# Kernel optimization log

Hardware: AMD Instinct MI355X
Metric: run time of the kernel (lower is better)

Reference implementation:

```python
import jax, jax.numpy as jnp
import numpy as np

H = 12          # num_heads
D = 32          # head_dim = dim // num_heads
C = H * D       # 384
SCALE = D ** -0.5


def _split2(y, B, N):
    # y: [B, N, 2*C] -> two tensors [B, H, N, D] (branch 1, branch 2)
    y = y.reshape(B, N, 2, H, D)
    return y[:, :, 0].transpose(0, 2, 1, 3), y[:, :, 1].transpose(0, 2, 1, 3)


def setup_inputs() -> dict:
    key = jax.random.key(0)
    ks = jax.random.split(key, 16)
    s = 0.02
    inp = {
        "x": jax.random.normal(ks[0], (8, 4096, C), jnp.float32),
        "attn": jax.random.normal(ks[1], (8, 4096, C), jnp.float32),
        "agent_input": jax.random.normal(ks[2], (8, 64, C), jnp.float32),
        # Linear weights stored as [in, out] (jax convention)
        "Wq_lf": jax.random.normal(ks[3], (C, 2 * C), jnp.float32) * s,
        "bq_lf": jnp.zeros((2 * C,), jnp.float32),
        "Wk_ag": jax.random.normal(ks[4], (C, 2 * C), jnp.float32) * s,
        "bk_ag": jnp.zeros((2 * C,), jnp.float32),
        "wa": jax.random.normal(ks[5], (2,), jnp.float32) * 0.5,   # mlp_attn_a Linear(2,1) weight
        "ba": jnp.zeros((1,), jnp.float32),
        "Wq_ag": jax.random.normal(ks[6], (C, 2 * C), jnp.float32) * s,
        "bq_ag": jnp.zeros((2 * C,), jnp.float32),
        "Wk_hf": jax.random.normal(ks[7], (C, 2 * C), jnp.float32) * s,
        "bk_hf": jnp.zeros((2 * C,), jnp.float32),
        "Wv_hf": jax.random.normal(ks[8], (C, C), jnp.float32) * s,
        "bv_hf": jnp.zeros((C,), jnp.float32),
        "wb": jax.random.normal(ks[9], (2,), jnp.float32) * 0.5,   # mlp_attn_b Linear(2,1) weight
        "bb": jnp.zeros((1,), jnp.float32),
        "Wproj": jax.random.normal(ks[10], (C, C), jnp.float32) * s,
        "bproj": jnp.zeros((C,), jnp.float32),
    }
    return inp


def reference(x, attn, agent_input, Wq_lf, bq_lf, Wk_ag, bk_ag, wa, ba,
              Wq_ag, bq_ag, Wk_hf, bk_hf, Wv_hf, bv_hf, wb, bb, Wproj, bproj):
    B, N, _ = x.shape
    Na = agent_input.shape[1]
    # --- branch A: pixel queries vs agent keys ---
    q1, q2 = _split2(x @ Wq_lf + bq_lf, B, N)              # [B,H,N,D] x2
    k1, k2 = _split2(agent_input @ Wk_ag + bk_ag, B, Na)   # [B,H,Na,D] x2
    s1 = jnp.einsum('bhnd,bhmd->bhnm', q1, k1) * SCALE     # [B,H,N,Na]
    s2 = jnp.einsum('bhnd,bhmd->bhnm', q2, k2) * SCALE
    # Linear(2,1) fusion of stacked scores, then softmax over agents
    attn_agent = jax.nn.softmax(s1 * wa[0] + s2 * wa[1] + ba[0], axis=-1)
    # --- branch B: agent queries vs high-freq keys/values ---
    qa1, qa2 = _split2(agent_input @ Wq_ag + bq_ag, B, Na)  # [B,H,Na,D] x2
    kh1, kh2 = _split2(attn @ Wk_hf + bk_hf, B, N)          # [B,H,N,D] x2
    v = (attn @ Wv_hf + bv_hf).reshape(B, N, H, D).transpose(0, 2, 1, 3)  # [B,H,N,D]
    t1 = jnp.einsum('bhmd,bhnd->bhmn', qa1, kh1) * SCALE    # [B,H,Na,N]
    t2 = jnp.einsum('bhmd,bhnd->bhmn', qa2, kh2) * SCALE
    attn_v = jax.nn.softmax(t1 * wb[0] + t2 * wb[1] + bb[0], axis=-1)
    x_s = attn_v @ v                 # [B,H,Na,D]
    x_out = attn_agent @ x_s         # [B,H,N,D]
    x_out = x_out.transpose(0, 2, 1, 3).reshape(B, N, H * D)
    return x_out @ Wproj + bproj
```

## Files before the change

kernel.cpp:

```cpp
#include <hip/hip_runtime.h>

#define KB 8
#define KN 4096
#define KNA 64
#define KH 12
#define KD 32
#define KC 384
#define KC2 768
#define KSCALE 0.17677669529663688f
#define NCH 16

typedef __bf16 bf16x8 __attribute__((ext_vector_type(8)));
typedef float  f32x4  __attribute__((ext_vector_type(4)));

static __device__ __forceinline__ unsigned short f2bf(float f) {
    unsigned int u = __builtin_bit_cast(unsigned int, f);
    u += 0x7FFFu + ((u >> 16) & 1u);
    return (unsigned short)(u >> 16);
}
static __device__ __forceinline__ float bf2f(unsigned short h) {
    return __builtin_bit_cast(float, (unsigned int)h << 16);
}

static __device__ __forceinline__ void gld_lds16(const unsigned short* g, unsigned short* l) {
    __builtin_amdgcn_global_load_lds(
        (const __attribute__((address_space(1))) unsigned int*)g,
        (__attribute__((address_space(3))) unsigned int*)l, 16, 0, 0);
}

#define MFMA_16x16x32 __builtin_amdgcn_mfma_f32_16x16x32_bf16

__global__ __launch_bounds__(256) void k_transpose(
    const float* __restrict__ Win, float* __restrict__ Wout)
{
    __shared__ float tile[32][33];
    const int tx = threadIdx.x, ty = threadIdx.y;
    const int j0 = blockIdx.x * 32, c0 = blockIdx.y * 32;
    #pragma unroll
    for (int yy = 0; yy < 4; ++yy)
        tile[ty + yy*8][tx] = Win[(size_t)(c0 + ty + yy*8)*KC2 + j0 + tx];
    __syncthreads();
    #pragma unroll
    for (int yy = 0; yy < 4; ++yy)
        Wout[(size_t)(j0 + ty + yy*8)*KC + c0 + tx] = tile[tx][ty + yy*8];
}

__global__ __launch_bounds__(256) void k_tcastT(
    const float* __restrict__ src, unsigned short* __restrict__ dstT,
    unsigned short* __restrict__ dstRM,
    int R, int C, long sstride, long dTstride, long dRMstride)
{
    __shared__ unsigned short lds[64][80];
    const int t = threadIdx.x;
    const int r0 = blockIdx.x * 64, c0 = blockIdx.y * 64;
    const float* s = src + (size_t)blockIdx.z * sstride;
    #pragma unroll
    for (int i = 0; i < 16; ++i) {
        int f = t + i*256; int rr = f >> 6, cc = f & 63;
        lds[rr][cc] = f2bf(s[(size_t)(r0+rr)*C + c0 + cc]);
    }
    __syncthreads();
    if (dstT) {
        unsigned short* dT = dstT + (size_t)blockIdx.z * dTstride;
        #pragma unroll
        for (int i = 0; i < 8; ++i) {
            int o = t + i*256;
            int chunk = o >> 10, c = (o >> 4) & 63, pair = o & 15;
            int r = chunk*32 + pair*2;
            unsigned int v = (unsigned int)lds[r][c] | ((unsigned int)lds[r+1][c] << 16);
            size_t off = ((size_t)((r0>>5) + chunk)*C + c0 + c)*32 + pair*2;
            *reinterpret_cast<unsigned int*>(dT + off) = v;
        }
    }
    if (dstRM) {
        unsigned short* dR = dstRM + (size_t)blockIdx.z * dRMstride;
        #pragma unroll
        for (int i = 0; i < 2; ++i) {
            int idx = t*2 + i;
            int n = idx >> 3, gt = idx & 7;
            int g = (c0 >> 3) + gt;
            int slot = g ^ ((r0 + n) & 7);
            *reinterpret_cast<bf16x8*>(dR + (size_t)(r0+n)*C + slot*8) =
                *reinterpret_cast<const bf16x8*>(&lds[n][gt*8]);
        }
    }
}

__global__ __launch_bounds__(256) void k_tcastHL(
    const float* __restrict__ src, unsigned short* __restrict__ dstHi,
    unsigned short* __restrict__ dstLo)
{
    __shared__ unsigned short lh[64][80];
    __shared__ unsigned short ll[64][80];
    const int t = threadIdx.x;
    const int r0 = blockIdx.x * 64, c0 = blockIdx.y * 64;
    #pragma unroll
    for (int i = 0; i < 16; ++i) {
        int f = t + i*256; int rr = f >> 6, cc = f & 63;
        float v = src[(size_t)(r0+rr)*KC2 + c0 + cc];
        unsigned short h = f2bf(v);
        lh[rr][cc] = h;
        ll[rr][cc] = f2bf(v - bf2f(h));
    }
    __syncthreads();
    #pragma unroll
    for (int i = 0; i < 8; ++i) {
        int o = t + i*256;
        int chunk = o >> 10, c = (o >> 4) & 63, pair = o & 15;
        int r = chunk*32 + pair*2;
        unsigned int vh = (unsigned int)lh[r][c] | ((unsigned int)lh[r+1][c] << 16);
        unsigned int vl = (unsigned int)ll[r][c] | ((unsigned int)ll[r+1][c] << 16);
        size_t off = ((size_t)((r0>>5) + chunk)*KC2 + c0 + c)*32 + pair*2;
        *reinterpret_cast<unsigned int*>(dstHi + off) = vh;
        *reinterpret_cast<unsigned int*>(dstLo + off) = vl;
    }
}

__global__ __launch_bounds__(512, 1) void k_agproj2(
    const float* __restrict__ agent,
    const unsigned short* __restrict__ KHi, const unsigned short* __restrict__ KLo,
    const unsigned short* __restrict__ QHi, const unsigned short* __restrict__ QLo,
    const float* __restrict__ bk_ag, const float* __restrict__ bq_ag,
    float* __restrict__ Kag, float* __restrict__ Qa)
{
    extern __shared__ char smem[];
    unsigned short* aHi = (unsigned short*)smem;
    unsigned short* aLo = (unsigned short*)(smem + 49152);
    const int tid = threadIdx.x;
    const int wid = tid >> 6, lane = tid & 63;
    const int tx = lane & 15, ty = lane >> 4;
    const int rt = blockIdx.x, wsel = blockIdx.y, z = blockIdx.z;
    const unsigned short* WHi = wsel ? QHi : KHi;
    const unsigned short* WLo = wsel ? QLo : KLo;
    const float* bias = wsel ? bq_ag : bk_ag;
    float* dst = wsel ? Qa : Kag;

    {
        const float4* s4 = reinterpret_cast<const float4*>(agent + (size_t)rt*64*KC);
        #pragma unroll
        for (int i = 0; i < 12; ++i) {
            int f = tid + i*512;
            int n = f / 96, c4 = f % 96;
            float4 v = s4[f];
            ushort4 h4, l4;
            h4.x = f2bf(v.x); l4.x = f2bf(v.x - bf2f(h4.x));
            h4.y = f2bf(v.y); l4.y = f2bf(v.y - bf2f(h4.y));
            h4.z = f2bf(v.z); l4.z = f2bf(v.z - bf2f(h4.z));
            h4.w = f2bf(v.w); l4.w = f2bf(v.w - bf2f(h4.w));
            int g = c4 >> 1, half = c4 & 1;
            int gs = g ^ (n & 7);
            *reinterpret_cast<ushort4*>(aHi + n*384 + gs*8 + half*4) = h4;
            *reinterpret_cast<ushort4*>(aLo + n*384 + gs*8 + half*4) = l4;
        }
    }
    f32x4 acc[4][3];
    #pragma unroll
    for (int i = 0; i < 4; ++i)
        #pragma unroll
        for (int j = 0; j < 3; ++j) acc[i][j] = (f32x4){0.f,0.f,0.f,0.f};
    __syncthreads();

    #pragma unroll
    for (int kk = 0; kk < 12; ++kk) {
        bf16x8 ah[4], al[4];
        #pragma unroll
        for (int ng = 0; ng < 4; ++ng) {
            int n = ng*16 + tx;
            int gs = (kk*4 + ty) ^ (n & 7);
            ah[ng] = *reinterpret_cast<const bf16x8*>(aHi + n*384 + gs*8);
            al[ng] = *reinterpret_cast<const bf16x8*>(aLo + n*384 + gs*8);
        }
        #pragma unroll
        for (int cs = 0; cs < 3; ++cs) {
            int col = z*KC + wid*48 + cs*16 + tx;
            bf16x8 bh = *reinterpret_cast<const bf16x8*>(WHi + ((size_t)kk*KC2 + col)*32 + ty*8);
            bf16x8 bl = *reinterpret_cast<const bf16x8*>(WLo + ((size_t)kk*KC2 + col)*32 + ty*8);
            #pragma unroll
            for (int ng = 0; ng < 4; ++ng) {
                acc[ng][cs] = MFMA_16x16x32(ah[ng], bh, acc[ng][cs], 0, 0, 0);
                acc[ng][cs] = MFMA_16x16x32(ah[ng], bl, acc[ng][cs], 0, 0, 0);
                acc[ng][cs] = MFMA_16x16x32(al[ng], bh, acc[ng][cs], 0, 0, 0);
            }
        }
    }
    #pragma unroll
    for (int cs = 0; cs < 3; ++cs) {
        int col = z*KC + wid*48 + cs*16 + tx;
        float bv = bias[col];
        #pragma unroll
        for (int ng = 0; ng < 4; ++ng)
            #pragma unroll
            for (int r = 0; r < 4; ++r) {
                int row = rt*64 + ng*16 + ty*4 + r;
                dst[(size_t)row*KC2 + col] = acc[ng][cs][r] + bv;
            }
    }
}

__global__ __launch_bounds__(128) void k_build_F(
    const float* __restrict__ WkT, const float* __restrict__ Qa,
    const float* __restrict__ wb, unsigned short* __restrict__ Fbf)
{
    __shared__ float q_lds[8][64];
    const int tid = threadIdx.x;
    const int g = blockIdx.x;
    const int b = blockIdx.y;
    const int h = (g*8) >> 6;
    const float t0 = KSCALE*wb[0], t1 = KSCALE*wb[1];
    #pragma unroll
    for (int l = 0; l < 4; ++l) {
        int v = tid + l*128;
        int i = v >> 6, d = v & 63;
        int m = (g*8 + i) & 63;
        int jj = (d < KD) ? (h*KD + d) : (KC + h*KD + d - KD);
        float cf = (d < KD) ? t0 : t1;
        q_lds[i][d] = cf * Qa[(size_t)(b*KNA + m)*KC2 + jj];
    }
    __syncthreads();
    float acc[8][3] = {};
    for (int d = 0; d < 64; ++d) {
        int row = (d < KD) ? (h*KD + d) : (KC + h*KD + d - KD);
        const float* wr = WkT + (size_t)row*KC;
        float w0 = wr[tid], w1 = wr[tid+128], w2 = wr[tid+256];
        #pragma unroll
        for (int i = 0; i < 8; ++i) {
            float q = q_lds[i][d];
            acc[i][0] = fmaf(q, w0, acc[i][0]);
            acc[i][1] = fmaf(q, w1, acc[i][1]);
            acc[i][2] = fmaf(q, w2, acc[i][2]);
        }
    }
    #pragma unroll
    for (int i = 0; i < 8; ++i)
        #pragma unroll
        for (int l = 0; l < 3; ++l)
            Fbf[((size_t)b*KC2 + g*8 + i)*KC + tid + l*128] = f2bf(acc[i][l]);
}

__global__ __launch_bounds__(256) void k_kabc(
    const float* __restrict__ Kag, const float* __restrict__ Qa,
    const float* __restrict__ wa, const float* __restrict__ bk_hf,
    const float* __restrict__ wb, const float* __restrict__ bbv,
    unsigned short* __restrict__ KA, float* __restrict__ cB)
{
    const int b = blockIdx.x, tid = threadIdx.x;
    const float s0 = KSCALE * wa[0], s1 = KSCALE * wa[1];
    #pragma unroll
    for (int i = 0; i < 24; ++i) {
        int v = tid + i*256;
        int w = v >> 8, m = (v >> 2) & 63, k8 = v & 3;
        float sc = (w >= 12) ? s1 : s0;
        const float* sp = Kag + ((size_t)(b*KNA + m))*KC2 + w*32 + k8*8;
        float4 f0 = *reinterpret_cast<const float4*>(sp);
        float4 f1 = *reinterpret_cast<const float4*>(sp + 4);
        ushort4 h0 = { f2bf(f0.x*sc), f2bf(f0.y*sc), f2bf(f0.z*sc), f2bf(f0.w*sc) };
        ushort4 h1 = { f2bf(f1.x*sc), f2bf(f1.y*sc), f2bf(f1.z*sc), f2bf(f1.w*sc) };
        unsigned short* dp = KA + ((size_t)(b*24 + w)*64 + m)*32 + k8*8;
        *reinterpret_cast<ushort4*>(dp)     = h0;
        *reinterpret_cast<ushort4*>(dp + 4) = h1;
    }
    const float t0 = KSCALE*wb[0], t1 = KSCALE*wb[1];
    for (int hm = tid; hm < KC2; hm += 256) {
        int h = hm >> 6, m = hm & 63;
        const float* qp = Qa + (size_t)(b*KNA + m)*KC2;
        float bb2 = 0.f;
        for (int d = 0; d < KD; ++d)
            bb2 += t0*bk_hf[h*KD+d]*qp[h*KD+d] + t1*bk_hf[KC+h*KD+d]*qp[KC+h*KD+d];
        cB[(size_t)b*KC2 + hm] = bb2 + bbv[0];
    }
}

__global__ __launch_bounds__(512, 4) void k_vproj2(
    const float* __restrict__ attn, const unsigned short* __restrict__ WvT2,
    const float* __restrict__ bv, unsigned short* __restrict__ Abf,
    unsigned short* __restrict__ Vt2)
{
    extern __shared__ char smem[];
    unsigned short* a_rm = (unsigned short*)smem;
    const int tid = threadIdx.x;
    const int wid = tid >> 6, lane = tid & 63;
    const int tx = lane & 15, ty = lane >> 4;
    const int nb = blockIdx.x, b = blockIdx.y;
    const int wn = wid >> 2, wd = wid & 3;

    {
        const float4* src = reinterpret_cast<const float4*>(attn + ((size_t)(b*KN + nb*64))*KC);
        unsigned short* ab = Abf + ((size_t)(b*KN + nb*64))*KC;
        #pragma unroll
        for (int i = 0; i < 12; ++i) {
            int f = tid + i*512;
            int n = f / 96, c4 = f % 96;
            float4 v = src[f];
            ushort4 h4 = { f2bf(v.x), f2bf(v.y), f2bf(v.z), f2bf(v.w) };
            int g = c4 >> 1, half = c4 & 1;
            int gs = g ^ (n & 7);
            *reinterpret_cast<ushort4*>(a_rm + n*384 + gs*8 + half*4) = h4;
            *reinterpret_cast<ushort4*>(ab + (size_t)n*384 + gs*8 + half*4) = h4;
        }
    }
    f32x4 acc[2][6];
    #pragma unroll
    for (int i = 0; i < 2; ++i)
        #pragma unroll
        for (int j = 0; j < 6; ++j) acc[i][j] = (f32x4){0.f,0.f,0.f,0.f};
    __syncthreads();

    #pragma unroll
    for (int kk = 0; kk < 12; ++kk) {
        bf16x8 af[2];
        #pragma unroll
        for (int ns = 0; ns < 2; ++ns) {
            int n = wn*32 + ns*16 + tx;
            int gs = (kk*4 + ty) ^ (n & 7);
            af[ns] = *reinterpret_cast<const bf16x8*>(a_rm + n*384 + gs*8);
        }
        #pragma unroll
        for (int cs = 0; cs < 6; ++cs) {
            int d = wd*96 + cs*16 + tx;
            bf16x8 bf = *reinterpret_cast<const bf16x8*>(WvT2 + ((size_t)kk*KC + d)*32 + ty*8);
            #pragma unroll
            for (int ns = 0; ns < 2; ++ns)
                acc[ns][cs] = MFMA_16x16x32(af[ns], bf, acc[ns][cs], 0, 0, 0);
        }
    }
    #pragma unroll
    for (int cs = 0; cs < 6; ++cs) {
        int d = wd*96 + cs*16 + tx;
        float bvv = bv[d];
        #pragma unroll
        for (int ns = 0; ns < 2; ++ns) {
            ushort4 h4;
            h4.x = f2bf(acc[ns][cs][0] + bvv);
            h4.y = f2bf(acc[ns][cs][1] + bvv);
            h4.z = f2bf(acc[ns][cs][2] + bvv);
            h4.w = f2bf(acc[ns][cs][3] + bvv);
            size_t off = (((size_t)b*(KN>>5) + nb*2 + wn)*KC + d)*32 + ns*16 + ty*4;
            *reinterpret_cast<ushort4*>(Vt2 + off) = h4;
        }
    }
}

__global__ __launch_bounds__(512, 4) void k_flash3(
    const unsigned short* __restrict__ Abf, const unsigned short* __restrict__ Vt2,
    const unsigned short* __restrict__ Fbf, const float* __restrict__ cB,
    float* __restrict__ Vpart, float* __restrict__ lpart,
    int nchunk, int NK)
{
    extern __shared__ char smem[];
    unsigned short* a_rm = (unsigned short*)smem;
    unsigned short* p    = (unsigned short*)(smem + 49152);
    float*          redl = (float*)(smem + 58368);

    const int tid = threadIdx.x;
    const int wid = tid >> 6, lane = tid & 63;
    const int tx = lane & 15, ty = lane >> 4;
    const unsigned bid = blockIdx.x;
    const unsigned g = bid / KH;
    const int h = bid - g*KH;
    const int b = g / nchunk;
    const int chunk = g - b*nchunk;
    const int n0 = chunk * NK;
    const int wn = wid >> 2, wh = wid & 3;
    const int wph = wid >> 1, wpd = wid & 1;

    bf16x8 ffrag[12];
    {
        const unsigned short* fp = Fbf + ((size_t)(b*KC2 + h*64 + wh*16 + tx))*KC + ty*8;
        #pragma unroll
        for (int kk = 0; kk < 12; ++kk)
            ffrag[kk] = *reinterpret_cast<const bf16x8*>(fp + kk*32);
    }
    const float cbv = cB[(size_t)b*KC2 + h*64 + wh*16 + tx];
    float lacc = 0.f;
    f32x4 Vacc = (f32x4){0.f,0.f,0.f,0.f};

    const unsigned short* atile = Abf + ((size_t)b*KN + n0)*KC;
    #pragma unroll
    for (int i = 0; i < 6; ++i)
        gld_lds16(atile + (size_t)tid*8 + i*4096, a_rm + tid*8 + i*4096);
    __syncthreads();

    const int NT = NK >> 6;
    for (int nt = 0; nt < NT; ++nt) {
        size_t vrow = (size_t)b*(KN >> 5) + ((n0 + nt*64) >> 5);
        bf16x8 vf0 = *reinterpret_cast<const bf16x8*>(
            Vt2 + ((vrow + 0)*KC + h*KD + wpd*16 + tx)*32 + ty*8);
        bf16x8 vf1 = *reinterpret_cast<const bf16x8*>(
            Vt2 + ((vrow + 1)*KC + h*KD + wpd*16 + tx)*32 + ty*8);
        f32x4 tacc[2];
        tacc[0] = (f32x4){0.f,0.f,0.f,0.f};
        tacc[1] = (f32x4){0.f,0.f,0.f,0.f};
        __builtin_amdgcn_s_setprio(1);
        #pragma unroll
        for (int kk = 0; kk < 12; ++kk) {
            #pragma unroll
            for (int ns = 0; ns < 2; ++ns) {
                int n = wn*32 + ns*16 + tx;
                int gs = (kk*4 + ty) ^ (n & 7);
                bf16x8 af = *reinterpret_cast<const bf16x8*>(a_rm + n*384 + gs*8);
                tacc[ns] = MFMA_16x16x32(af, ffrag[kk], tacc[ns], 0, 0, 0);
            }
        }
        __builtin_amdgcn_s_setprio(0);
        #pragma unroll
        for (int ns = 0; ns < 2; ++ns) {
            float e0 = __expf(tacc[ns][0] + cbv);
            float e1 = __expf(tacc[ns][1] + cbv);
            float e2 = __expf(tacc[ns][2] + cbv);
            float e3 = __expf(tacc[ns][3] + cbv);
            lacc += e0 + e1 + e2 + e3;
            int hm = wh*16 + tx;
            int np = wn*32 + ns*16 + ty*4;
            ushort4 h4 = { f2bf(e0), f2bf(e1), f2bf(e2), f2bf(e3) };
            *reinterpret_cast<ushort4*>(p + hm*72 + np) = h4;
        }
        __syncthreads();
        if (nt + 1 < NT) {
            const unsigned short* at = atile + (size_t)(nt+1)*64*KC;
            #pragma unroll
            for (int i = 0; i < 6; ++i)
                gld_lds16(at + (size_t)tid*8 + i*4096, a_rm + tid*8 + i*4096);
        }
        bf16x8 pa0 = *reinterpret_cast<const bf16x8*>(p + (wph*16 + tx)*72 + 0*32 + ty*8);
        bf16x8 pa1 = *reinterpret_cast<const bf16x8*>(p + (wph*16 + tx)*72 + 1*32 + ty*8);
        Vacc = MFMA_16x16x32(pa0, vf0, Vacc, 0, 0, 0);
        Vacc = MFMA_16x16x32(pa1, vf1, Vacc, 0, 0, 0);
        __syncthreads();
    }
    #pragma unroll
    for (int r = 0; r < 4; ++r)
        Vpart[(((size_t)(b*KH + h)*nchunk + chunk)*64 + wph*16 + ty*4 + r)*32 + wpd*16 + tx]
            = Vacc[r];
    lacc += __shfl_xor(lacc, 16);
    lacc += __shfl_xor(lacc, 32);
    if (lane < 16) redl[wn*64 + wh*16 + tx] = lacc;
    __syncthreads();
    if (tid < 64)
        lpart[((size_t)b*KC2 + h*64 + tid)*nchunk + chunk] = redl[tid] + redl[64 + tid];
}

__global__ __launch_bounds__(384) void k_combine4(
    const float* __restrict__ Vpart, const float* __restrict__ lpart,
    const float* __restrict__ Wproj, unsigned short* __restrict__ Mt2)
{
    __shared__ float xs[16][32];
    __shared__ float lred[16][NCH];
    __shared__ float invl[16];
    const int h = blockIdx.x, b = blockIdx.y, q = blockIdx.z;
    const int tid = threadIdx.x;
    if (tid < 16*NCH) {
        int hm_l = tid >> 4, ch = tid & (NCH-1);
        lred[hm_l][ch] = lpart[((size_t)b*KC2 + h*64 + q*16 + hm_l)*NCH + ch];
    }
    __syncthreads();
    if (tid < 16) {
        float s = 0.f;
        #pragma unroll
        for (int j = 0; j < NCH; ++j) s += lred[tid][j];
        invl[tid] = 1.f / s;
    }
    __syncthreads();
    for (int v = tid; v < 512; v += 384) {
        int hm_l = v >> 5, d = v & 31;
        const float* vp = Vpart + (((size_t)(b*KH + h)*NCH)*64 + q*16 + hm_l)*32 + d;
        float u = 0.f;
        #pragma unroll
        for (int ch = 0; ch < NCH; ++ch) u += vp[(size_t)ch*2048];
        xs[hm_l][d] = u * invl[hm_l];
    }
    __syncthreads();
    const int e = tid;
    float wp[32];
    #pragma unroll
    for (int d = 0; d < 32; ++d) wp[d] = Wproj[(size_t)(h*KD + d)*KC + e];
    ushort4 line[4];
    #pragma unroll
    for (int mq = 0; mq < 4; ++mq) {
        float a4[4];
        #pragma unroll
        for (int mr = 0; mr < 4; ++mr) {
            float a = 0.f;
            #pragma unroll
            for (int d = 0; d < 32; ++d)
                a = fmaf(xs[mq*4 + mr][d], wp[d], a);
            a4[mr] = a;
        }
        line[mq] = (ushort4){ f2bf(a4[0]), f2bf(a4[1]), f2bf(a4[2]), f2bf(a4[3]) };
    }
    unsigned short* dst = Mt2 + (((size_t)(b*KH + h)*2 + (q >> 1))*KC + e)*32 + (q & 1)*16;
    #pragma unroll
    for (int mq = 0; mq < 4; ++mq)
        *reinterpret_cast<ushort4*>(dst + mq*4) = line[mq];
}

__global__ __launch_bounds__(512, 4) void k_qkproj(
    const float* __restrict__ src, const unsigned short* __restrict__ WT2,
    const float* __restrict__ bias, unsigned short* __restrict__ dstAf)
{
    extern __shared__ char smem[];
    unsigned short* xb = (unsigned short*)smem;
    const int tid = threadIdx.x;
    const int wid = tid >> 6, lane = tid & 63;
    const int tx = lane & 15, ty = lane >> 4;
    const int nb = blockIdx.x, b = blockIdx.y, z = blockIdx.z;

    {
        const float4* s4 = reinterpret_cast<const float4*>(src + ((size_t)(b*KN + nb*64))*KC);
        #pragma unroll
        for (int i = 0; i < 12; ++i) {
            int f = tid + i*512;
            int n = f / 96, c4 = f % 96;
            float4 v = s4[f];
            ushort4 h4 = { f2bf(v.x), f2bf(v.y), f2bf(v.z), f2bf(v.w) };
            int g = c4 >> 1, half = c4 & 1;
            int gs = g ^ (n & 7);
            *reinterpret_cast<ushort4*>(xb + n*384 + gs*8 + half*4) = h4;
        }
    }
    f32x4 acc[4][3];
    #pragma unroll
    for (int i = 0; i < 4; ++i)
        #pragma unroll
        for (int j = 0; j < 3; ++j) acc[i][j] = (f32x4){0.f,0.f,0.f,0.f};
    __syncthreads();

    #pragma unroll
    for (int kk = 0; kk < 12; ++kk) {
        bf16x8 af[4];
        #pragma unroll
        for (int ng = 0; ng < 4; ++ng) {
            int n = ng*16 + tx;
            int gs = (kk*4 + ty) ^ (n & 7);
            af[ng] = *reinterpret_cast<const bf16x8*>(xb + n*384 + gs*8);
        }
        #pragma unroll
        for (int cs = 0; cs < 3; ++cs) {
            int col = z*KC + wid*48 + cs*16 + tx;
            bf16x8 bf = *reinterpret_cast<const bf16x8*>(WT2 + ((size_t)kk*KC2 + col)*32 + ty*8);
            #pragma unroll
            for (int ng = 0; ng < 4; ++ng)
                acc[ng][cs] = MFMA_16x16x32(af[ng], bf, acc[ng][cs], 0, 0, 0);
        }
    }
    #pragma unroll
    for (int cs = 0; cs < 3; ++cs) {
        int col = z*KC + wid*48 + cs*16 + tx;
        float bv = bias[col];
        int w = col >> 5, tyq = (col >> 3) & 3, j = col & 7;
        #pragma unroll
        for (int ng = 0; ng < 4; ++ng) {
            int nt = nb*4 + ng;
            size_t base = ((((size_t)(b*256 + nt)*24 + w)*4 + tyq)*16)*8 + j;
            #pragma unroll
            for (int r = 0; r < 4; ++r) {
                int row = ty*4 + r;
                dstAf[base + (size_t)row*8] = f2bf(acc[ng][cs][r] + bv);
            }
        }
    }
}

__global__ __launch_bounds__(512, 4) void k_out5(
    const unsigned short* __restrict__ QAf, const unsigned short* __restrict__ KA,
    const float* __restrict__ ba, const unsigned short* __restrict__ Mt2,
    const float* __restrict__ bproj, float* __restrict__ out)
{
    extern __shared__ char smem[];
    unsigned short* p0 = (unsigned short*)smem;
    unsigned short* p1 = (unsigned short*)(smem + 17920);

    const int tid = threadIdx.x;
    const int wid = tid >> 6, lane = tid & 63;
    const int tx = lane & 15, ty = lane >> 4;
    const int nb = blockIdx.x, b = blockIdx.y;
    const int hq2 = wid >> 2, wn = wid & 3;
    const int es = wid * 48;
    const float ba0 = ba[0];

    f32x4 oacc[4][3];
    #pragma unroll
    for (int i = 0; i < 4; ++i)
        #pragma unroll
        for (int j = 0; j < 3; ++j) oacc[i][j] = (f32x4){0.f,0.f,0.f,0.f};

    for (int it = 0; it < 6; ++it) {
        unsigned short* pb = (it & 1) ? p1 : p0;
        const int hq = it*2 + hq2;
        const unsigned short* ap = QAf +
            (((size_t)(b*256 + nb*4 + wn)*24 + hq))*512 + (size_t)lane*8;
        bf16x8 a0 = *reinterpret_cast<const bf16x8*>(ap);
        bf16x8 a1 = *reinterpret_cast<const bf16x8*>(ap + 12*512);
        f32x4 tacc[4];
        #pragma unroll
        for (int s = 0; s < 4; ++s) tacc[s] = (f32x4){0.f,0.f,0.f,0.f};
        __builtin_amdgcn_s_setprio(1);
        #pragma unroll
        for (int s = 0; s < 4; ++s) {
            bf16x8 kb0 = *reinterpret_cast<const bf16x8*>(
                KA + ((size_t)(b*24 + hq)*64 + s*16 + tx)*32 + ty*8);
            bf16x8 kb1 = *reinterpret_cast<const bf16x8*>(
                KA + ((size_t)(b*24 + 12 + hq)*64 + s*16 + tx)*32 + ty*8);
            tacc[s] = MFMA_16x16x32(a0, kb0, tacc[s], 0, 0, 0);
            tacc[s] = MFMA_16x16x32(a1, kb1, tacc[s], 0, 0, 0);
        }
        __builtin_amdgcn_s_setprio(0);
        float e[4][4];
        float ls[4] = {0.f, 0.f, 0.f, 0.f};
        #pragma unroll
        for (int s = 0; s < 4; ++s)
            #pragma unroll
            for (int r = 0; r < 4; ++r) {
                e[s][r] = __expf(tacc[s][r] + ba0);
                ls[r] += e[s][r];
            }
        #pragma unroll
        for (int mask = 1; mask < 16; mask <<= 1)
            #pragma unroll
            for (int r = 0; r < 4; ++r)
                ls[r] += __shfl_xor(ls[r], mask);
        float inv[4];
        #pragma unroll
        for (int r = 0; r < 4; ++r) inv[r] = 1.f / ls[r];
        #pragma unroll
        for (int s = 0; s < 4; ++s)
            #pragma unroll
            for (int r = 0; r < 4; ++r) {
                int n = wn*16 + ty*4 + r;
                pb[n*140 + hq2*64 + s*16 + tx] = f2bf(e[s][r] * inv[r]);
            }
        __syncthreads();
        __builtin_amdgcn_s_setprio(1);
        #pragma unroll
        for (int ks = 0; ks < 4; ++ks) {
            const int hM = it*2 + (ks >> 1);
            const int inner = ks & 1;
            bf16x8 pa[4];
            #pragma unroll
            for (int ng = 0; ng < 4; ++ng)
                pa[ng] = *reinterpret_cast<const bf16x8*>(
                    pb + (ng*16 + tx)*140 + ks*32 + ty*8);
            #pragma unroll
            for (int j = 0; j < 3; ++j) {
                bf16x8 mf = *reinterpret_cast<const bf16x8*>(
                    Mt2 + (((size_t)(b*KH + hM)*2 + inner)*KC + es + j*16 + tx)*32 + ty*8);
                #pragma unroll
                for (int ng = 0; ng < 4; ++ng)
                    oacc[ng][j] = MFMA_16x16x32(pa[ng], mf, oacc[ng][j], 0, 0, 0);
            }
        }
        __builtin_amdgcn_s_setprio(0);
    }
    float bp[3];
    #pragma unroll
    for (int j = 0; j < 3; ++j) bp[j] = bproj[es + j*16 + tx];
    #pragma unroll
    for (int ng = 0; ng < 4; ++ng)
        #pragma unroll
        for (int r = 0; r < 4; ++r) {
            size_t base = (size_t)(b*KN + nb*64 + ng*16 + ty*4 + r)*KC;
            #pragma unroll
            for (int j = 0; j < 3; ++j)
                out[base + es + j*16 + tx] = oacc[ng][j][r] + bp[j];
        }
}

extern "C" void kernel_launch(void* const* d_in, const int* in_sizes, int n_in,
                              void* d_out, int out_size, void* d_ws, size_t ws_size,
                              hipStream_t stream) {
    const float* x     = (const float*)d_in[0];
    const float* attn  = (const float*)d_in[1];
    const float* agent = (const float*)d_in[2];
    const float* Wq_lf = (const float*)d_in[3];
    const float* bq_lf = (const float*)d_in[4];
    const float* Wk_ag = (const float*)d_in[5];
    const float* bk_ag = (const float*)d_in[6];
    const float* wa    = (const float*)d_in[7];
    const float* ba    = (const float*)d_in[8];
    const float* Wq_ag = (const float*)d_in[9];
    const float* bq_ag = (const float*)d_in[10];
    const float* Wk_hf = (const float*)d_in[11];
    const float* bk_hf = (const float*)d_in[12];
    const float* Wv_hf = (const float*)d_in[13];
    const float* bv_hf = (const float*)d_in[14];
    const float* wb    = (const float*)d_in[15];
    const float* bb    = (const float*)d_in[16];
    const float* Wproj = (const float*)d_in[17];
    const float* bproj = (const float*)d_in[18];
    float* out = (float*)d_out;
    float* ws  = (float*)d_ws;

    const size_t o_Kag  = 0;
    const size_t o_Qa   = 393216;
    const size_t o_cB   = 792576;
    const size_t o_Fbf  = 798720;
    const size_t o_WkT  = 1978368;
    const size_t o_WvT2 = 2273280;
    const size_t o_WqT2 = 2310144;
    const size_t o_KA   = 2457600;
    const size_t o_Mt2  = 2654208;
    const size_t o_Abf  = 3833856;
    const size_t o_Vt2  = 6979584;
    const size_t o_lp   = 13271040;
    const size_t o_Vp   = 13467648;
    const size_t o_QAf  = 3833856;
    const size_t o_KHi  = o_Abf;
    const size_t o_KLo  = o_Abf + 147456;
    const size_t o_QHi  = o_Abf + 294912;
    const size_t o_QLo  = o_Abf + 442368;
    (void)ws_size; (void)in_sizes; (void)n_in; (void)out_size;

    unsigned short* Fbf  = (unsigned short*)(ws + o_Fbf);
    unsigned short* WvT2 = (unsigned short*)(ws + o_WvT2);
    unsigned short* WqT2 = (unsigned short*)(ws + o_WqT2);
    unsigned short* KA   = (unsigned short*)(ws + o_KA);
    unsigned short* Mt2  = (unsigned short*)(ws + o_Mt2);
    unsigned short* Abf  = (unsigned short*)(ws + o_Abf);
    unsigned short* Vt2  = (unsigned short*)(ws + o_Vt2);
    unsigned short* QAf  = (unsigned short*)(ws + o_QAf);
    unsigned short* KHi  = (unsigned short*)(ws + o_KHi);
    unsigned short* KLo  = (unsigned short*)(ws + o_KLo);
    unsigned short* QHi  = (unsigned short*)(ws + o_QHi);
    unsigned short* QLo  = (unsigned short*)(ws + o_QLo);

    const int ap_lds = 98304;
    const int vp_lds = 49152;
    const int fl_lds = 58880;
    const int qp_lds = 49152;
    const int ko_lds = 35840;
    (void)hipFuncSetAttribute(reinterpret_cast<const void*>(k_agproj2),
                              hipFuncAttributeMaxDynamicSharedMemorySize, ap_lds);
    (void)hipFuncSetAttribute(reinterpret_cast<const void*>(k_vproj2),
                              hipFuncAttributeMaxDynamicSharedMemorySize, vp_lds);
    (void)hipFuncSetAttribute(reinterpret_cast<const void*>(k_flash3),
                              hipFuncAttributeMaxDynamicSharedMemorySize, fl_lds);
    (void)hipFuncSetAttribute(reinterpret_cast<const void*>(k_qkproj),
                              hipFuncAttributeMaxDynamicSharedMemorySize, qp_lds);
    (void)hipFuncSetAttribute(reinterpret_cast<const void*>(k_out5),
                              hipFuncAttributeMaxDynamicSharedMemorySize, ko_lds);

    k_tcastHL<<<dim3(6, 12), 256, 0, stream>>>(Wk_ag, KHi, KLo);
    k_tcastHL<<<dim3(6, 12), 256, 0, stream>>>(Wq_ag, QHi, QLo);
    k_agproj2<<<dim3(8, 2, 2), 512, ap_lds, stream>>>(
        agent, KHi, KLo, QHi, QLo, bk_ag, bq_ag, ws + o_Kag, ws + o_Qa);
    k_transpose<<<dim3(24, 12), dim3(32, 8), 0, stream>>>(Wk_hf, ws + o_WkT);
    k_tcastT<<<dim3(6, 12, 1), 256, 0, stream>>>(Wq_lf, WqT2, nullptr,
                                                 KC, KC2, 0, 0, 0);
    k_tcastT<<<dim3(6, 6, 1), 256, 0, stream>>>(Wv_hf, WvT2, nullptr,
                                                 KC, KC, 0, 0, 0);
    k_kabc<<<dim3(KB), 256, 0, stream>>>(ws + o_Kag, ws + o_Qa, wa, bk_hf, wb, bb,
                                         KA, ws + o_cB);
    k_build_F<<<dim3(96, 8), 128, 0, stream>>>(ws + o_WkT, ws + o_Qa, wb, Fbf);

    k_vproj2<<<dim3(KN/64, KB), 512, vp_lds, stream>>>(attn, WvT2, bv_hf, Abf, Vt2);

    k_flash3<<<dim3(KH * KB * NCH), 512, fl_lds, stream>>>(
        Abf, Vt2, Fbf, ws + o_cB, ws + o_Vp, ws + o_lp, NCH, KN / NCH);
    k_combine4<<<dim3(KH, KB, 4), 384, 0, stream>>>(
        ws + o_Vp, ws + o_lp, Wproj, Mt2);
    k_qkproj<<<dim3(KN/64, KB, 2), 512, qp_lds, stream>>>(x, WqT2, bq_lf, QAf);
    k_out5<<<dim3(KN/64, KB), 512, ko_lds, stream>>>(
        QAf, KA, ba, Mt2, bproj, out);
}
```

Measured before the change: 263.7 us.

## Fuse query projection into output kernel, keep projected queries in LDS

```diff
diff --git a/kernel.cpp b/kernel.cpp
--- a/kernel.cpp
+++ b/kernel.cpp
@@ -493,19 +493,26 @@
         *reinterpret_cast<ushort4*>(dst + mq*4) = line[mq];
 }
 
-__global__ __launch_bounds__(512, 4) void k_qkproj(
-    const float* __restrict__ src, const unsigned short* __restrict__ WT2,
-    const float* __restrict__ bias, unsigned short* __restrict__ dstAf)
+__global__ __launch_bounds__(512, 1) void k_fused(
+    const float* __restrict__ x, const unsigned short* __restrict__ WT2,
+    const float* __restrict__ bq, const unsigned short* __restrict__ KA,
+    const float* __restrict__ ba, const unsigned short* __restrict__ Mt2,
+    const float* __restrict__ bproj, float* __restrict__ out)
 {
     extern __shared__ char smem[];
     unsigned short* xb = (unsigned short*)smem;
+    unsigned short* p0 = (unsigned short*)smem;
+    unsigned short* p1 = (unsigned short*)(smem + 17920);
+    unsigned short* qf = (unsigned short*)(smem + 49152);
+
     const int tid = threadIdx.x;
     const int wid = tid >> 6, lane = tid & 63;
     const int tx = lane & 15, ty = lane >> 4;
-    const int nb = blockIdx.x, b = blockIdx.y, z = blockIdx.z;
+    const int nb = blockIdx.x, b = blockIdx.y;
+    const float ba0 = ba[0];
 
     {
-        const float4* s4 = reinterpret_cast<const float4*>(src + ((size_t)(b*KN + nb*64))*KC);
+        const float4* s4 = reinterpret_cast<const float4*>(x + ((size_t)(b*KN + nb*64))*KC);
         #pragma unroll
         for (int i = 0; i < 12; ++i) {
             int f = tid + i*512;
@@ -517,65 +524,51 @@
             *reinterpret_cast<ushort4*>(xb + n*384 + gs*8 + half*4) = h4;
         }
     }
-    f32x4 acc[4][3];
-    #pragma unroll
-    for (int i = 0; i < 4; ++i)
-        #pragma unroll
-        for (int j = 0; j < 3; ++j) acc[i][j] = (f32x4){0.f,0.f,0.f,0.f};
-    __syncthreads();
-
-    #pragma unroll
-    for (int kk = 0; kk < 12; ++kk) {
-        bf16x8 af[4];
-        #pragma unroll
-        for (int ng = 0; ng < 4; ++ng) {
-            int n = ng*16 + tx;
-            int gs = (kk*4 + ty) ^ (n & 7);
-            af[ng] = *reinterpret_cast<const bf16x8*>(xb + n*384 + gs*8);
+    __syncthreads();
+
+    #pragma unroll
+    for (int z = 0; z < 2; ++z) {
+        f32x4 acc[4][3];
+        #pragma unroll
+        for (int i = 0; i < 4; ++i)
+            #pragma unroll
+            for (int j = 0; j < 3; ++j) acc[i][j] = (f32x4){0.f,0.f,0.f,0.f};
+        #pragma unroll
+        for (int kk = 0; kk < 12; ++kk) {
+            bf16x8 af[4];
+            #pragma unroll
+            for (int ng = 0; ng < 4; ++ng) {
+                int n = ng*16 + tx;
+                int gs = (kk*4 + ty) ^ (n & 7);
+                af[ng] = *reinterpret_cast<const bf16x8*>(xb + n*384 + gs*8);
+            }
+            #pragma unroll
+            for (int cs = 0; cs < 3; ++cs) {
+                int col = z*KC + wid*48 + cs*16 + tx;
+                bf16x8 bf = *reinterpret_cast<const bf16x8*>(
+                    WT2 + ((size_t)kk*KC2 + col)*32 + ty*8);
+                #pragma unroll
+                for (int ng = 0; ng < 4; ++ng)
+                    acc[ng][cs] = MFMA_16x16x32(af[ng], bf, acc[ng][cs], 0, 0, 0);
+            }
         }
         #pragma unroll
         for (int cs = 0; cs < 3; ++cs) {
             int col = z*KC + wid*48 + cs*16 + tx;
-            bf16x8 bf = *reinterpret_cast<const bf16x8*>(WT2 + ((size_t)kk*KC2 + col)*32 + ty*8);
+            float bv = bq[col];
+            int w = col >> 5, tyq = (col >> 3) & 3, j = col & 7;
             #pragma unroll
             for (int ng = 0; ng < 4; ++ng)
-                acc[ng][cs] = MFMA_16x16x32(af[ng], bf, acc[ng][cs], 0, 0, 0);
-        }
-    }
-    #pragma unroll
-    for (int cs = 0; cs < 3; ++cs) {
-        int col = z*KC + wid*48 + cs*16 + tx;
-        float bv = bias[col];
-        int w = col >> 5, tyq = (col >> 3) & 3, j = col & 7;
-        #pragma unroll
-        for (int ng = 0; ng < 4; ++ng) {
-            int nt = nb*4 + ng;
-            size_t base = ((((size_t)(b*256 + nt)*24 + w)*4 + tyq)*16)*8 + j;
-            #pragma unroll
-            for (int r = 0; r < 4; ++r) {
-                int row = ty*4 + r;
-                dstAf[base + (size_t)row*8] = f2bf(acc[ng][cs][r] + bv);
-            }
-        }
-    }
-}
-
-__global__ __launch_bounds__(512, 4) void k_out5(
-    const unsigned short* __restrict__ QAf, const unsigned short* __restrict__ KA,
-    const float* __restrict__ ba, const unsigned short* __restrict__ Mt2,
-    const float* __restrict__ bproj, float* __restrict__ out)
-{
-    extern __shared__ char smem[];
-    unsigned short* p0 = (unsigned short*)smem;
-    unsigned short* p1 = (unsigned short*)(smem + 17920);
-
-    const int tid = threadIdx.x;
-    const int wid = tid >> 6, lane = tid & 63;
-    const int tx = lane & 15, ty = lane >> 4;
-    const int nb = blockIdx.x, b = blockIdx.y;
+                #pragma unroll
+                for (int r = 0; r < 4; ++r)
+                    qf[(((ng*24 + w)*4 + tyq)*16 + ty*4 + r)*8 + j] =
+                        f2bf(acc[ng][cs][r] + bv);
+        }
+    }
+    __syncthreads();
+
     const int hq2 = wid >> 2, wn = wid & 3;
     const int es = wid * 48;
-    const float ba0 = ba[0];
 
     f32x4 oacc[4][3];
     #pragma unroll
@@ -586,8 +579,7 @@
     for (int it = 0; it < 6; ++it) {
         unsigned short* pb = (it & 1) ? p1 : p0;
         const int hq = it*2 + hq2;
-        const unsigned short* ap = QAf +
-            (((size_t)(b*256 + nb*4 + wn)*24 + hq))*512 + (size_t)lane*8;
+        const unsigned short* ap = qf + (size_t)(wn*24 + hq)*512 + lane*8;
         bf16x8 a0 = *reinterpret_cast<const bf16x8*>(ap);
         bf16x8 a1 = *reinterpret_cast<const bf16x8*>(ap + 12*512);
         f32x4 tacc[4];
@@ -702,7 +694,6 @@
     const size_t o_Vt2  = 6979584;
     const size_t o_lp   = 13271040;
     const size_t o_Vp   = 13467648;
-    const size_t o_QAf  = 3833856;
     const size_t o_KHi  = o_Abf;
     const size_t o_KLo  = o_Abf + 147456;
     const size_t o_QHi  = o_Abf + 294912;
@@ -716,7 +707,6 @@
     unsigned short* Mt2  = (unsigned short*)(ws + o_Mt2);
     unsigned short* Abf  = (unsigned short*)(ws + o_Abf);
     unsigned short* Vt2  = (unsigned short*)(ws + o_Vt2);
-    unsigned short* QAf  = (unsigned short*)(ws + o_QAf);
     unsigned short* KHi  = (unsigned short*)(ws + o_KHi);
     unsigned short* KLo  = (unsigned short*)(ws + o_KLo);
     unsigned short* QHi  = (unsigned short*)(ws + o_QHi);
@@ -725,18 +715,15 @@
     const int ap_lds = 98304;
     const int vp_lds = 49152;
     const int fl_lds = 58880;
-    const int qp_lds = 49152;
-    const int ko_lds = 35840;
+    const int fu_lds = 147456;
     (void)hipFuncSetAttribute(reinterpret_cast<const void*>(k_agproj2),
                               hipFuncAttributeMaxDynamicSharedMemorySize, ap_lds);
     (void)hipFuncSetAttribute(reinterpret_cast<const void*>(k_vproj2),
                               hipFuncAttributeMaxDynamicSharedMemorySize, vp_lds);
     (void)hipFuncSetAttribute(reinterpret_cast<const void*>(k_flash3),
                               hipFuncAttributeMaxDynamicSharedMemorySize, fl_lds);
-    (void)hipFuncSetAttribute(reinterpret_cast<const void*>(k_qkproj),
-                              hipFuncAttributeMaxDynamicSharedMemorySize, qp_lds);
-    (void)hipFuncSetAttribute(reinterpret_cast<const void*>(k_out5),
-                              hipFuncAttributeMaxDynamicSharedMemorySize, ko_lds);
+    (void)hipFuncSetAttribute(reinterpret_cast<const void*>(k_fused),
+                              hipFuncAttributeMaxDynamicSharedMemorySize, fu_lds);
 
     k_tcastHL<<<dim3(6, 12), 256, 0, stream>>>(Wk_ag, KHi, KLo);
     k_tcastHL<<<dim3(6, 12), 256, 0, stream>>>(Wq_ag, QHi, QLo);
@@ -757,7 +744,6 @@
         Abf, Vt2, Fbf, ws + o_cB, ws + o_Vp, ws + o_lp, NCH, KN / NCH);
     k_combine4<<<dim3(KH, KB, 4), 384, 0, stream>>>(
         ws + o_Vp, ws + o_lp, Wproj, Mt2);
-    k_qkproj<<<dim3(KN/64, KB, 2), 512, qp_lds, stream>>>(x, WqT2, bq_lf, QAf);
-    k_out5<<<dim3(KN/64, KB), 512, ko_lds, stream>>>(
-        QAf, KA, ba, Mt2, bproj, out);
-}
+    k_fused<<<dim3(KN/64, KB), 512, fu_lds, stream>>>(
+        x, WqT2, bq_lf, KA, ba, Mt2, bproj, out);
+}
```

After: 260.3 us. About the same (-1.3%).
